# Optimization experiments

Measured on AMD Instinct MI355X. Metric: run time of the kernel, lower is better.

Reference implementation:

```python
import jax, jax.numpy as jnp
import numpy as np

B, N_IN, N_OUT, N_NODES, N_EDGES = 64, 128, 256, 20000, 320000
ITERS, LEAK, IN_AMP, OUT_AMP = 150, 0.01, 1.2, 1.2


def setup_inputs() -> dict:
    key = jax.random.key(0)
    ks = jax.random.split(key, 8)
    x = jax.random.normal(ks[0], (B, N_IN), dtype=jnp.float32)
    # projection weights (inputAmplitude / projectionAmplitude * ones)
    in_w = IN_AMP * jnp.ones((N_IN,), dtype=jnp.float32)
    out_w = OUT_AMP * jnp.ones((N_OUT,), dtype=jnp.float32)
    rec_w = 0.1 + 0.1 * jax.random.uniform(ks[1], (N_EDGES,), dtype=jnp.float32)
    inhib = jax.random.bernoulli(ks[2], 0.3, (N_EDGES,))
    rec_w = jnp.where(inhib, -rec_w, rec_w)
    biases = 0.001 * jnp.ones((N_NODES, 1), dtype=jnp.float32)
    rows = jax.random.randint(ks[3], (N_EDGES,), 0, N_NODES)
    cols = jax.random.randint(ks[4], (N_EDGES,), 0, N_NODES)
    in_idx = jax.random.randint(ks[5], (N_IN,), 0, N_NODES)
    out_idx = jax.random.randint(ks[6], (N_OUT,), 0, N_NODES)
    return {"x": x, "in_w": in_w, "out_w": out_w, "rec_w": rec_w,
            "biases": biases, "rows": rows, "cols": cols,
            "in_idx": in_idx, "out_idx": out_idx}


def reference(x, in_w, out_w, rec_w, biases, rows, cols, in_idx, out_idx):
    n_nodes = biases.shape[0]

    def mml_act(v):
        # leaky below 0, Michaelis-Menten-like saturation above 0.5
        v = jnp.where(v < 0, v * LEAK, v)
        return jnp.where(v > 0.5, 1.0 - 0.25 / v, v)

    def spmv(h):
        # A @ h with A in COO form: out[r] += w_e * h[c]
        msg = rec_w[:, None] * h[cols]                      # [E, B]
        return jax.ops.segment_sum(msg, rows, num_segments=n_nodes)

    # input projection: scatter weighted inputs into node vector
    y = jnp.zeros((x.shape[0], n_nodes), x.dtype).at[:, in_idx].set(in_w * x)
    b_in = y.T + biases                                      # [N, B]

    def step(h, _):
        return mml_act(spmv(h) + b_in), None

    h0 = jnp.zeros_like(b_in)
    hT, _ = jax.lax.scan(step, h0, None, length=ITERS)
    xhat = hT.T                                              # [B, N]
    return out_w * xhat[:, out_idx]                          # [B, n_out]
```

## Files before the change

kernel.cpp:

```cpp
#include <hip/hip_runtime.h>
#include <hip/hip_fp16.h>

#define N_NODES 20000
#define N_EDGES 320000
#define BATCH   64
#define N_IN    128
#define N_OUT   256
#define CAP     64
#define ITERS   150
#define LEAK    0.01f

#define CNT_MASK 0x3FFFFFFF
#define FLAG_BIT (1 << 30)

#define NSLICE 32
#define BPS    8
#define NPB    2500
#define NT     1024
#define NBLK   (NSLICE * BPS)
#define SLICE_U32 20480
#define SLICE_U128 (SLICE_U32 / 4)
#define OWN_U128  625
#define PAIRS  32
#define CTR_STRIDE 32

typedef unsigned int uint;
typedef unsigned long long ull;
typedef _Float16 h2_t __attribute__((ext_vector_type(2)));
typedef uint u32x4 __attribute__((ext_vector_type(4)));

#define AT_LDI(p)    __hip_atomic_load((const int*)(p), __ATOMIC_RELAXED, __HIP_MEMORY_SCOPE_AGENT)
#define AT_ADDI(p,v) __hip_atomic_fetch_add((int*)(p), (v), __ATOMIC_RELAXED, __HIP_MEMORY_SCOPE_AGENT)

__device__ __forceinline__ void st128_mall(u32x4* p, u32x4 v) {
    asm volatile("global_store_dwordx4 %0, %1, off sc0 sc1"
                 :: "v"(p), "v"(v) : "memory");
}

__device__ __forceinline__ float fdot2u(uint w, uint h, float acc) {
    union { uint u; h2_t h; } a, b; a.u = w; b.u = h;
    return __builtin_amdgcn_fdot2(a.h, b.h, acc, false);
}

__global__ void setup_kernel(uint* __restrict__ hGA, uint* __restrict__ hGB,
                             int* __restrict__ cnt,
                             uint* __restrict__ colpair, uint* __restrict__ wpair,
                             int* __restrict__ mctr) {
    int idx = blockIdx.x * blockDim.x + threadIdx.x;
    int stride = gridDim.x * blockDim.x;
    for (int i = idx; i < NSLICE * SLICE_U32; i += stride) { hGA[i] = 0u; hGB[i] = 0u; }
    for (int i = idx; i < N_NODES; i += stride) cnt[i] = 0;
    for (int i = idx; i < PAIRS * N_NODES; i += stride) { colpair[i] = 0u; wpair[i] = 0u; }
    for (int i = idx; i < NSLICE * CTR_STRIDE; i += stride) mctr[i] = 0;
}

__global__ void input_scatter_kernel(float* __restrict__ bin,
                                     const float* __restrict__ x,
                                     const float* __restrict__ in_w,
                                     const int* __restrict__ in_idx,
                                     const float* __restrict__ biases,
                                     int* __restrict__ cnt) {
    int i = blockIdx.x;
    int b = threadIdx.x;
    int node = in_idx[i];
    if (b == 0) atomicOr(&cnt[node], FLAG_BIT);
    for (int j = i + 1; j < N_IN; j++)
        if (in_idx[j] == node) return;
    bin[node * BATCH + b] = biases[node] + in_w[i] * x[b * N_IN + i];
}

__global__ void ell_build_kernel(const int* __restrict__ rows,
                                 const int* __restrict__ cols,
                                 const float* __restrict__ rec_w,
                                 uint* __restrict__ colpair, uint* __restrict__ wpair,
                                 int* __restrict__ cnt) {
    int e = blockIdx.x * blockDim.x + threadIdx.x;
    if (e >= N_EDGES) return;
    int r = rows[e];
    int s = atomicAdd(&cnt[r], 1) & CNT_MASK;
    if (s < CAP) {
        int p = s >> 1, sh = (s & 1) * 16;
        atomicOr(&colpair[(size_t)p * N_NODES + r], (uint)cols[e] << sh);
        uint hw = (uint)__half_as_ushort(__float2half(rec_w[e]));
        atomicOr(&wpair[(size_t)p * N_NODES + r], hw << sh);
    }
}

__global__ __launch_bounds__(NT) void sort_kernel(const int* __restrict__ cnt,
                                                  int* __restrict__ permG,
                                                  int* __restrict__ rankOf) {
    __shared__ int hist[65], off[65];
    int nbase = blockIdx.x * NPB;
    int tid = threadIdx.x;
    if (tid < 65) hist[tid] = 0;
    __syncthreads();
    for (int r = tid; r < NPB; r += NT) {
        int c = cnt[nbase + r] & CNT_MASK; if (c > CAP) c = CAP;
        atomicAdd(&hist[c], 1);
    }
    __syncthreads();
    if (tid == 0) {
        int run = 0;
        for (int c = CAP; c >= 0; c--) { off[c] = run; run += hist[c]; }
    }
    __syncthreads();
    for (int r = tid; r < NPB; r += NT) {
        int c = cnt[nbase + r] & CNT_MASK; if (c > CAP) c = CAP;
        int rk = atomicAdd(&off[c], 1);
        permG[nbase + rk] = nbase + r;
        rankOf[nbase + r] = nbase + rk;
    }
}

__global__ void reorder_kernel(const uint* __restrict__ colpair,
                               const uint* __restrict__ wpair,
                               const int* __restrict__ permG,
                               const int* __restrict__ rankOf,
                               uint2* __restrict__ cwR) {
    int r = blockIdx.x * blockDim.x + threadIdx.x;
    int p = blockIdx.y;
    if (r >= N_NODES) return;
    size_t o = (size_t)p * N_NODES;
    int n = permG[r];
    uint cc = colpair[o + n];
    uint lo = (uint)rankOf[cc & 0xFFFFu];
    uint hi = (uint)rankOf[cc >> 16];
    cwR[o + r] = make_uint2(lo | (hi << 16), wpair[o + n]);
}

__device__ __forceinline__ uint finish_node(float a0, float a1, float b0, float b1) {
    float r0 = b0 + a0, r1 = b1 + a1;
    float u0 = (r0 < 0.f) ? r0 * LEAK : r0;
    float u1 = (r1 < 0.f) ? r1 * LEAK : r1;
    float v0 = (u0 > 0.5f) ? (1.0f - 0.25f / u0) : u0;
    float v1 = (u1 > 0.5f) ? (1.0f - 0.25f / u1) : u1;
    union { __half2 h; uint u; } p;
    p.h = __halves2half2(__float2half(v0), __float2half(v1));
    return p.u;
}

__device__ __forceinline__ void hoist_consts(
        int nbase, int tid, int s,
        const int* __restrict__ cnt, const int* __restrict__ permG,
        const float* __restrict__ bin, const float* __restrict__ biases,
        int* rank, float* mb0, float* mb1, bool* ma, int& kp) {
    int kmax = 0;
#pragma unroll
    for (int j = 0; j < 3; j++) {
        int sl = 3 * tid + j;
        ma[j] = (sl < NPB);
        rank[j] = nbase + (ma[j] ? sl : 0);
        int n = permG[rank[j]];
        int cv = cnt[n];
        int c = cv & CNT_MASK; if (c > CAP) c = CAP;
        if (ma[j] && c > kmax) kmax = c;
        if (cv & FLAG_BIT) {
            mb0[j] = bin[(size_t)n * BATCH + 2 * s];
            mb1[j] = bin[(size_t)n * BATCH + 2 * s + 1];
        } else {
            float bb = biases[n]; mb0[j] = bb; mb1[j] = bb;
        }
    }
    kp = (kmax + 1) >> 1;
}

__device__ __forceinline__ void compute_pairs(
        const int* rank, int kp,
        const uint2* __restrict__ cwR,
        const uint* __restrict__ lds_h, float* a0, float* a1) {
    a0[0] = a0[1] = a0[2] = 0.f;
    a1[0] = a1[1] = a1[2] = 0.f;
#pragma unroll 2
    for (int p = 0; p < kp; p++) {
        size_t o = (size_t)p * N_NODES;
#pragma unroll
        for (int j = 0; j < 3; j++) {
            uint2 m = cwR[o + rank[j]];
            uint ha = lds_h[m.x & 0xFFFFu];
            uint hb = lds_h[m.x >> 16];
            uint lo = __builtin_amdgcn_perm(hb, ha, 0x05040100u);
            uint hi = __builtin_amdgcn_perm(hb, ha, 0x07060302u);
            a0[j] = fdot2u(m.y, lo, a0[j]);
            a1[j] = fdot2u(m.y, hi, a1[j]);
        }
    }
}

__global__ __launch_bounds__(NT) void persistent_kernel(
        uint* hGA, uint* hGB,
        const float* __restrict__ bin, const float* __restrict__ biases,
        const uint2* __restrict__ cwR,
        const int* __restrict__ cnt, const int* __restrict__ permG,
        int* mctr) {
    extern __shared__ uint lds_h[];
    int bid = blockIdx.x, tid = threadIdx.x;
    int s = bid >> 3, sub = bid & 7;
    int nbase = sub * NPB;

    int rank[3]; float mb0[3], mb1[3]; bool ma[3]; int kp;
    hoist_consts(nbase, tid, s, cnt, permG, bin, biases, rank, mb0, mb1, ma, kp);

    for (int i = tid; i < SLICE_U32; i += NT) lds_h[i] = 0u;
    __syncthreads();

    uint* hA_s = hGA + (size_t)s * SLICE_U32;
    uint* hB_s = hGB + (size_t)s * SLICE_U32;
    int* mc = &mctr[s * CTR_STRIDE];

    for (int t = 0; t < ITERS; t++) {
        uint* hout = (t & 1) ? hB_s : hA_s;

        float a0[3], a1[3];
        compute_pairs(rank, kp, cwR, lds_h, a0, a1);
        uint v[3];
#pragma unroll
        for (int j = 0; j < 3; j++) v[j] = finish_node(a0[j], a1[j], mb0[j], mb1[j]);

        __syncthreads();
#pragma unroll
        for (int j = 0; j < 3; j++)
            if (ma[j]) lds_h[rank[j]] = v[j];
        __syncthreads();

        if (tid < OWN_U128) {
            int i = sub * OWN_U128 + tid;
            st128_mall((u32x4*)hout + i, ((const u32x4*)lds_h)[i]);
        }
        if (t == ITERS - 1) break;

        __syncthreads();
        if (tid == 0) {
            AT_ADDI(mc, 1);
            int target = BPS * (t + 1);
            while (AT_LDI(mc) < target) __builtin_amdgcn_s_sleep(2);
        }
        __syncthreads();

        {
            const u32x4* src = (const u32x4*)hout;
            u32x4* dst = (u32x4*)lds_h;
            int i0 = tid, i1 = tid + NT, i2 = tid + 2 * NT,
                i3 = tid + 3 * NT, i4 = tid + 4 * NT;
            u32x4 v0, v1, v2, v3, v4;
            asm volatile(
                "global_load_dwordx4 %0, %5, off sc0 sc1\n\t"
                "global_load_dwordx4 %1, %6, off sc0 sc1\n\t"
                "global_load_dwordx4 %2, %7, off sc0 sc1\n\t"
                "global_load_dwordx4 %3, %8, off sc0 sc1\n\t"
                "global_load_dwordx4 %4, %9, off sc0 sc1\n\t"
                "s_waitcnt vmcnt(0)"
                : "=&v"(v0), "=&v"(v1), "=&v"(v2), "=&v"(v3), "=&v"(v4)
                : "v"(src + i0), "v"(src + i1), "v"(src + i2),
                  "v"(src + i3), "v"(src + i4)
                : "memory");
            dst[i0] = v0; dst[i1] = v1; dst[i2] = v2; dst[i3] = v3; dst[i4] = v4;
        }
        __syncthreads();
    }
}

__global__ __launch_bounds__(NT) void step_kernel(
        const uint* __restrict__ hprev, uint* __restrict__ hnext,
        const float* __restrict__ bin, const float* __restrict__ biases,
        const uint2* __restrict__ cwR,
        const int* __restrict__ cnt, const int* __restrict__ permG) {
    extern __shared__ uint lds_h[];
    int bid = blockIdx.x, tid = threadIdx.x;
    int s = bid >> 3, sub = bid & 7;
    int nbase = sub * NPB;

    int rank[3]; float mb0[3], mb1[3]; bool ma[3]; int kp;
    hoist_consts(nbase, tid, s, cnt, permG, bin, biases, rank, mb0, mb1, ma, kp);

    const uint* hp = hprev + (size_t)s * SLICE_U32;
    for (int i = tid; i < SLICE_U32; i += NT) lds_h[i] = hp[i];
    __syncthreads();

    float a0[3], a1[3];
    compute_pairs(rank, kp, cwR, lds_h, a0, a1);
    uint* ho = hnext + (size_t)s * SLICE_U32;
#pragma unroll
    for (int j = 0; j < 3; j++)
        if (ma[j]) ho[rank[j]] = finish_node(a0[j], a1[j], mb0[j], mb1[j]);
}

__global__ void output_kernel(const uint* __restrict__ hfinal,
                              const int* __restrict__ out_idx,
                              const int* __restrict__ rankOf,
                              const float* __restrict__ out_w,
                              float* __restrict__ out) {
    int o = threadIdx.x;
    int b = blockIdx.x;
    uint v = hfinal[(size_t)(b >> 1) * SLICE_U32 + rankOf[out_idx[o]]];
    unsigned short h = (b & 1) ? (unsigned short)(v >> 16) : (unsigned short)(v & 0xFFFF);
    out[b * N_OUT + o] = out_w[o] * __half2float(__ushort_as_half(h));
}

extern "C" void kernel_launch(void* const* d_in, const int* in_sizes, int n_in,
                              void* d_out, int out_size, void* d_ws, size_t ws_size,
                              hipStream_t stream) {
    const float* x      = (const float*)d_in[0];
    const float* in_w   = (const float*)d_in[1];
    const float* out_w  = (const float*)d_in[2];
    const float* rec_w  = (const float*)d_in[3];
    const float* biases = (const float*)d_in[4];
    const int*   rows   = (const int*)d_in[5];
    const int*   cols   = (const int*)d_in[6];
    const int*   in_idx = (const int*)d_in[7];
    const int*   oidx   = (const int*)d_in[8];
    float* out = (float*)d_out;

    char* ws = (char*)d_ws;
    uint*  hGA     = (uint*)ws;  ws += (size_t)NSLICE * SLICE_U32 * 4;
    uint*  hGB     = (uint*)ws;  ws += (size_t)NSLICE * SLICE_U32 * 4;
    float* bin     = (float*)ws; ws += (size_t)N_NODES * BATCH * 4;
    uint*  colpair = (uint*)ws;  ws += (size_t)PAIRS * N_NODES * 4;
    uint*  wpair   = (uint*)ws;  ws += (size_t)PAIRS * N_NODES * 4;
    uint2* cwR     = (uint2*)ws; ws += (size_t)PAIRS * N_NODES * 8;
    int*   cnt     = (int*)ws;   ws += (size_t)N_NODES * 4;
    int*   permG   = (int*)ws;   ws += (size_t)N_NODES * 4;
    int*   rankOf  = (int*)ws;   ws += (size_t)N_NODES * 4;
    int*   mctr    = (int*)ws;   ws += (size_t)NSLICE * CTR_STRIDE * 4;

    const int shmem = SLICE_U32 * 4;
    hipFuncSetAttribute((const void*)persistent_kernel,
                        hipFuncAttributeMaxDynamicSharedMemorySize, shmem);
    hipFuncSetAttribute((const void*)step_kernel,
                        hipFuncAttributeMaxDynamicSharedMemorySize, shmem);

    setup_kernel<<<2048, 256, 0, stream>>>(hGA, hGB, cnt, colpair, wpair, mctr);
    input_scatter_kernel<<<N_IN, BATCH, 0, stream>>>(bin, x, in_w, in_idx,
                                                     biases, cnt);
    ell_build_kernel<<<(N_EDGES + 255) / 256, 256, 0, stream>>>(rows, cols, rec_w,
                                                                colpair, wpair, cnt);
    sort_kernel<<<N_NODES / NPB, NT, 0, stream>>>(cnt, permG, rankOf);
    reorder_kernel<<<dim3((N_NODES + 255) / 256, PAIRS), 256, 0, stream>>>(
        colpair, wpair, permG, rankOf, cwR);

    void* args[] = { (void*)&hGA, (void*)&hGB, (void*)&bin, (void*)&biases,
                     (void*)&cwR, (void*)&cnt, (void*)&permG, (void*)&mctr };
    hipError_t ce = hipLaunchCooperativeKernel((void*)persistent_kernel,
                                               dim3(NBLK), dim3(NT),
                                               args, shmem, stream);
    const uint* hfinal;
    if (ce == hipSuccess) {
        hfinal = hGB;
    } else {
        uint* pa = hGA;
        uint* pb = hGB;
        for (int t = 0; t < ITERS; t++) {
            step_kernel<<<NBLK, NT, shmem, stream>>>(pa, pb, bin, biases,
                                                     cwR, cnt, permG);
            uint* tmp = pa; pa = pb; pb = tmp;
        }
        hfinal = pa;
    }

    output_kernel<<<BATCH, N_OUT, 0, stream>>>(hfinal, oidx, rankOf, out_w, out);
}
```

Before: 1.089 ms.

## Replace per-slice atomic barrier with per-block flag tags and per-wave-pair fetch

The atomic counter barrier across the 8 blocks of a slice is replaced by per-block monotonic tags. Each block publishes its iteration number, and each pair of waves polls only the one producer block whose 625-vector segment it copies into LDS, skipping its own segment. A wave can therefore start fetching as soon as its producer is ready instead of waiting for the slowest block, and no atomic RMW is needed. In exchange there are 7 pollers per block hitting memory, and correctness relies on sc0 sc1 store ordering making the data visible before the tag.

```diff
diff --git a/kernel.cpp b/kernel.cpp
--- a/kernel.cpp
+++ b/kernel.cpp
@@ -19,23 +19,30 @@
 #define NT     1024
 #define NBLK   (NSLICE * BPS)
 #define SLICE_U32 20480
-#define SLICE_U128 (SLICE_U32 / 4)
 #define OWN_U128  625
 #define PAIRS  32
-#define CTR_STRIDE 32
+#define TAG_STRIDE 32
 
 typedef unsigned int uint;
 typedef unsigned long long ull;
 typedef _Float16 h2_t __attribute__((ext_vector_type(2)));
 typedef uint u32x4 __attribute__((ext_vector_type(4)));
 
-#define AT_LDI(p)    __hip_atomic_load((const int*)(p), __ATOMIC_RELAXED, __HIP_MEMORY_SCOPE_AGENT)
-#define AT_ADDI(p,v) __hip_atomic_fetch_add((int*)(p), (v), __ATOMIC_RELAXED, __HIP_MEMORY_SCOPE_AGENT)
-
 __device__ __forceinline__ void st128_mall(u32x4* p, u32x4 v) {
     asm volatile("global_store_dwordx4 %0, %1, off sc0 sc1"
                  :: "v"(p), "v"(v) : "memory");
 }
+__device__ __forceinline__ void st32_mall(uint* p, uint v) {
+    asm volatile("global_store_dword %0, %1, off sc0 sc1"
+                 :: "v"(p), "v"(v) : "memory");
+}
+__device__ __forceinline__ uint ld32_mall(const uint* p) {
+    uint v;
+    asm volatile("global_load_dword %0, %1, off sc0 sc1\n\t"
+                 "s_waitcnt vmcnt(0)"
+                 : "=v"(v) : "v"(p) : "memory");
+    return v;
+}
 
 __device__ __forceinline__ float fdot2u(uint w, uint h, float acc) {
     union { uint u; h2_t h; } a, b; a.u = w; b.u = h;
@@ -45,13 +52,13 @@
 __global__ void setup_kernel(uint* __restrict__ hGA, uint* __restrict__ hGB,
                              int* __restrict__ cnt,
                              uint* __restrict__ colpair, uint* __restrict__ wpair,
-                             int* __restrict__ mctr) {
+                             uint* __restrict__ tags) {
     int idx = blockIdx.x * blockDim.x + threadIdx.x;
     int stride = gridDim.x * blockDim.x;
     for (int i = idx; i < NSLICE * SLICE_U32; i += stride) { hGA[i] = 0u; hGB[i] = 0u; }
     for (int i = idx; i < N_NODES; i += stride) cnt[i] = 0;
     for (int i = idx; i < PAIRS * N_NODES; i += stride) { colpair[i] = 0u; wpair[i] = 0u; }
-    for (int i = idx; i < NSLICE * CTR_STRIDE; i += stride) mctr[i] = 0;
+    for (int i = idx; i < NSLICE * BPS * TAG_STRIDE; i += stride) tags[i] = 0u;
 }
 
 __global__ void input_scatter_kernel(float* __restrict__ bin,
@@ -191,11 +198,13 @@
         const float* __restrict__ bin, const float* __restrict__ biases,
         const uint2* __restrict__ cwR,
         const int* __restrict__ cnt, const int* __restrict__ permG,
-        int* mctr) {
+        uint* tags) {
     extern __shared__ uint lds_h[];
     int bid = blockIdx.x, tid = threadIdx.x;
     int s = bid >> 3, sub = bid & 7;
     int nbase = sub * NPB;
+    const int wave = tid >> 6, lane = tid & 63;
+    const int sb = wave >> 1, half = wave & 1;
 
     int rank[3]; float mb0[3], mb1[3]; bool ma[3]; int kp;
     hoist_consts(nbase, tid, s, cnt, permG, bin, biases, rank, mb0, mb1, ma, kp);
@@ -205,7 +214,7 @@
 
     uint* hA_s = hGA + (size_t)s * SLICE_U32;
     uint* hB_s = hGB + (size_t)s * SLICE_U32;
-    int* mc = &mctr[s * CTR_STRIDE];
+    uint* mytag = &tags[(s * BPS + sub) * TAG_STRIDE];
 
     for (int t = 0; t < ITERS; t++) {
         uint* hout = (t & 1) ? hB_s : hA_s;
@@ -229,19 +238,19 @@
         if (t == ITERS - 1) break;
 
         __syncthreads();
-        if (tid == 0) {
-            AT_ADDI(mc, 1);
-            int target = BPS * (t + 1);
-            while (AT_LDI(mc) < target) __builtin_amdgcn_s_sleep(2);
-        }
-        __syncthreads();
-
-        {
-            const u32x4* src = (const u32x4*)hout;
-            u32x4* dst = (u32x4*)lds_h;
-            int i0 = tid, i1 = tid + NT, i2 = tid + 2 * NT,
-                i3 = tid + 3 * NT, i4 = tid + 4 * NT;
-            u32x4 v0, v1, v2, v3, v4;
+        if (tid == 0) st32_mall(mytag, (uint)(t + 1));
+
+        if (sb != sub) {
+            if (lane == 0) {
+                const uint* rt = &tags[(s * BPS + sb) * TAG_STRIDE];
+                while (ld32_mall(rt) < (uint)(t + 1)) __builtin_amdgcn_s_sleep(2);
+            }
+            const u32x4* sp = (const u32x4*)hout + sb * OWN_U128;
+            u32x4* dp = (u32x4*)lds_h + sb * OWN_U128;
+            int it0 = half * 64 + lane;
+            int it4 = it0 + 512;
+            int c4 = (it4 <= 624) ? it4 : 624;
+            u32x4 r0, r1, r2, r3, r4;
             asm volatile(
                 "global_load_dwordx4 %0, %5, off sc0 sc1\n\t"
                 "global_load_dwordx4 %1, %6, off sc0 sc1\n\t"
@@ -249,11 +258,13 @@
                 "global_load_dwordx4 %3, %8, off sc0 sc1\n\t"
                 "global_load_dwordx4 %4, %9, off sc0 sc1\n\t"
                 "s_waitcnt vmcnt(0)"
-                : "=&v"(v0), "=&v"(v1), "=&v"(v2), "=&v"(v3), "=&v"(v4)
-                : "v"(src + i0), "v"(src + i1), "v"(src + i2),
-                  "v"(src + i3), "v"(src + i4)
+                : "=&v"(r0), "=&v"(r1), "=&v"(r2), "=&v"(r3), "=&v"(r4)
+                : "v"(sp + it0), "v"(sp + it0 + 128), "v"(sp + it0 + 256),
+                  "v"(sp + it0 + 384), "v"(sp + c4)
                 : "memory");
-            dst[i0] = v0; dst[i1] = v1; dst[i2] = v2; dst[i3] = v3; dst[i4] = v4;
+            dp[it0] = r0; dp[it0 + 128] = r1; dp[it0 + 256] = r2;
+            dp[it0 + 384] = r3;
+            if (it4 <= 624) dp[it4] = r4;
         }
         __syncthreads();
     }
@@ -320,7 +331,7 @@
     int*   cnt     = (int*)ws;   ws += (size_t)N_NODES * 4;
     int*   permG   = (int*)ws;   ws += (size_t)N_NODES * 4;
     int*   rankOf  = (int*)ws;   ws += (size_t)N_NODES * 4;
-    int*   mctr    = (int*)ws;   ws += (size_t)NSLICE * CTR_STRIDE * 4;
+    uint*  tags    = (uint*)ws;  ws += (size_t)NSLICE * BPS * TAG_STRIDE * 4;
 
     const int shmem = SLICE_U32 * 4;
     hipFuncSetAttribute((const void*)persistent_kernel,
@@ -328,7 +339,7 @@
     hipFuncSetAttribute((const void*)step_kernel,
                         hipFuncAttributeMaxDynamicSharedMemorySize, shmem);
 
-    setup_kernel<<<2048, 256, 0, stream>>>(hGA, hGB, cnt, colpair, wpair, mctr);
+    setup_kernel<<<2048, 256, 0, stream>>>(hGA, hGB, cnt, colpair, wpair, tags);
     input_scatter_kernel<<<N_IN, BATCH, 0, stream>>>(bin, x, in_w, in_idx,
                                                      biases, cnt);
     ell_build_kernel<<<(N_EDGES + 255) / 256, 256, 0, stream>>>(rows, cols, rec_w,
@@ -338,7 +349,7 @@
         colpair, wpair, permG, rankOf, cwR);
 
     void* args[] = { (void*)&hGA, (void*)&hGB, (void*)&bin, (void*)&biases,
-                     (void*)&cwR, (void*)&cnt, (void*)&permG, (void*)&mctr };
+                     (void*)&cwR, (void*)&cnt, (void*)&permG, (void*)&tags };
     hipError_t ce = hipLaunchCooperativeKernel((void*)persistent_kernel,
                                                dim3(NBLK), dim3(NT),
                                                args, shmem, stream);
```

New measurement: 1.067 ms. -2.0%, faster.
